# Kernel tuning notes

Hardware: AMD Instinct MI355X
Metric: run time of the kernel (lower is better)

The kernel has to match this reference:

```python
import jax, jax.numpy as jnp
import numpy as np

FP, DP, K, S, B, T, H, ZD = 96, 28, 3, 4, 64, 8, 512, 2
CP = FP - DP + 1          # 69, valid cross-correlation output size
NP = CP * CP              # 4761 = num_pixels


def setup_inputs() -> dict:
    key = jax.random.key(0)
    ks = jax.random.split(key, 12)
    def rn(k, shape, s=0.02):
        return jax.random.normal(k, shape, jnp.float32) * s
    return {
        "frames": jax.random.uniform(ks[0], (S, B, T, FP, FP), jnp.float32),
        "conv_kernel": jax.random.uniform(ks[1], (S, B, K, DP, DP), jnp.float32),
        "eps": jax.random.normal(ks[2], (S, B, K, ZD), jnp.float32),
        "W1": rn(ks[3], (NP, H)), "b1": jnp.zeros((H,), jnp.float32),
        "Wm1": rn(ks[4], (H, H // 2)), "bm1": jnp.zeros((H // 2,), jnp.float32),
        "Wm2": rn(ks[5], (H // 2, ZD)), "bm2": jnp.zeros((ZD,), jnp.float32),
        "Ws1": rn(ks[6], (H, H // 2)), "bs1": jnp.zeros((H // 2,), jnp.float32),
        "Ws2": rn(ks[7], (H // 2, ZD)), "bs2": jnp.zeros((ZD,), jnp.float32),
        "timestep": 0,
    }


def _axis_weights(p, n):
    """Bilinear 1-D gather indices/weights with zero padding outside [0, n)."""
    p0 = jnp.floor(p)
    f = p - p0
    i0 = p0.astype(jnp.int32)
    i1 = i0 + 1
    w0 = jnp.where((i0 >= 0) & (i0 < n), 1.0 - f, 0.0)
    w1 = jnp.where((i1 >= 0) & (i1 < n), f, 0.0)
    return jnp.clip(i0, 0, n - 1), jnp.clip(i1, 0, n - 1), w0, w1


def _place_digit(digit, zw):
    """AT.digit_to_frame: place DPxDP digit into FPxFP frame at z_where (torch
    affine_grid/grid_sample, align_corners=False, zero padding). theta scale =
    FP/DP, translation = -z_where*FP/DP, i.e. in_coord = (FP/DP)*(out - zw)."""
    scale = FP / DP
    out_c = (2.0 * jnp.arange(FP, dtype=jnp.float32) + 1.0) / FP - 1.0  # (FP,)
    px = ((scale * (out_c - zw[0]) + 1.0) * DP - 1.0) * 0.5  # x source pix
    py = ((scale * (out_c - zw[1]) + 1.0) * DP - 1.0) * 0.5  # y source pix
    y0, y1, wy0, wy1 = _axis_weights(py, DP)
    x0, x1, wx0, wx1 = _axis_weights(px, DP)
    # separable bilinear: interp rows then cols
    tmp = wy0[:, None] * digit[y0, :] + wy1[:, None] * digit[y1, :]  # (FP,DP)
    return wx0[None, :] * tmp[:, x0] + wx1[None, :] * tmp[:, x1]     # (FP,FP)

_place_batch = jax.vmap(_place_digit)


def reference(frames, conv_kernel, eps, W1, b1, Wm1, bm1, Wm2, bm2,
              Ws1, bs1, Ws2, bs2, timestep):
    SB = S * B
    frame_left = frames[:, :, timestep]  # (S,B,FP,FP)
    means, stds, zs = [], [], []
    for k in range(K):
        # per-sample dynamic-kernel cross-correlation via grouped conv
        lhs = frame_left.reshape(1, SB, FP, FP)
        rhs = conv_kernel[:, :, k].reshape(SB, 1, DP, DP)
        conved = jax.lax.conv_general_dilated(
            lhs, rhs, (1, 1), 'VALID', feature_group_count=SB)  # (1,SB,CP,CP)
        scores = jax.nn.softmax(conved.reshape(S, B, NP), axis=-1)
        h = jax.nn.relu(scores @ W1 + b1)                       # (S,B,H)
        mean_k = jnp.tanh(jax.nn.relu(h @ Wm1 + bm1) @ Wm2 + bm2)
        std_k = jnp.exp(jax.nn.relu(h @ Ws1 + bs1) @ Ws2 + bs2)
        z_k = mean_k + std_k * eps[:, :, k]                     # rsample
        recon = _place_batch(conv_kernel[:, :, k].reshape(SB, DP, DP),
                             z_k.reshape(SB, ZD)).reshape(S, B, FP, FP)
        frame_left = frame_left - recon
        means.append(mean_k); stds.append(std_k); zs.append(z_k)
    q_mean = jnp.stack(means, 2)    # (S,B,K,2)
    q_std = jnp.stack(stds, 2)
    z_where = jnp.stack(zs, 2)
    return jnp.stack([q_mean, q_std, z_where], 0)  # (3,S,B,K,2)
```

## Files before the change

kernel.cpp:

```cpp
#include <hip/hip_runtime.h>
#include <hip/hip_bf16.h>
#include <math.h>

#define FPD 96
#define DPD 28
#define CPD 69
#define NPD 4761
#define KKC 3
#define SBN 256
#define TT 8
#define HD 512
#define ZDD 2
#define KPAD 4768
#define SPLITK 15
#define FRSH 104
#define CVS 76

typedef __attribute__((ext_vector_type(8))) short bf16x8;
typedef __attribute__((ext_vector_type(4))) float f32x4;
typedef _Float16 half_t;
typedef __attribute__((ext_vector_type(2))) _Float16 half2_t;

__device__ __forceinline__ float bf2f_lo(unsigned int u) {
    union { unsigned int i; float f; } v; v.i = u << 16; return v.f;
}
__device__ __forceinline__ float bf2f_hi(unsigned int u) {
    union { unsigned int i; float f; } v; v.i = u & 0xffff0000u; return v.f;
}
__device__ __forceinline__ half2_t u2h(unsigned int u) {
    union { unsigned int i; half2_t h; } v; v.i = u; return v.h;
}

__global__ __launch_bounds__(256) void wprep_kernel(
    const float* __restrict__ W1, const float* __restrict__ Wm1,
    const float* __restrict__ Ws1,
    ushort* __restrict__ W1T, ushort* __restrict__ WhidT)
{
    __shared__ ushort tile[64][65];
    const int t = threadIdx.x;
    const int ln = t & 63;
    const int lr = t >> 6;
    const int b = blockIdx.x;

    if (b < 600) {
        const int k0 = (b % 75) * 64;
        const int n0 = (b / 75) * 64;
        #pragma unroll
        for (int i = 0; i < 16; ++i) {
            int kk = k0 + lr + i * 4;
            float v = (kk < NPD) ? W1[(size_t)kk * HD + n0 + ln] : 0.f;
            __hip_bfloat16 h = __float2bfloat16(v);
            tile[lr + i * 4][ln] = *reinterpret_cast<ushort*>(&h);
        }
        __syncthreads();
        #pragma unroll
        for (int i = 0; i < 16; ++i) {
            int nn = lr + i * 4;
            int kk = k0 + ln;
            if (kk < KPAD)
                W1T[(size_t)(n0 + nn) * KPAD + kk] = tile[ln][nn];
        }
    } else {
        const int bb = b - 600;
        const int i0 = (bb & 7) * 64;
        const int r0 = (bb >> 3) * 64;
        #pragma unroll
        for (int rep = 0; rep < 16; ++rep) {
            int i = i0 + lr + rep * 4;
            int r = r0 + ln;
            const float* src = (r >= 256) ? Ws1 : Wm1;
            float v = src[(size_t)i * 256 + (r & 255)];
            __hip_bfloat16 h = __float2bfloat16(v);
            tile[lr + rep * 4][ln] = *reinterpret_cast<ushort*>(&h);
        }
        __syncthreads();
        #pragma unroll
        for (int rep = 0; rep < 16; ++rep) {
            int r = r0 + lr + rep * 4;
            WhidT[(size_t)r * 512 + i0 + ln] = tile[ln][lr + rep * 4];
        }
    }
}

__global__ __launch_bounds__(1024, 4) void conv_softmax_kernel(
    const float* __restrict__ frames, const int* __restrict__ tsp,
    float* __restrict__ frameL, const float* __restrict__ ck,
    const float* __restrict__ z_cur,
    ushort* __restrict__ e_buf, float* __restrict__ inv_denom, int k)
{
    __shared__ __align__(16) half_t fr[96 * FRSH];
    __shared__ __align__(16) half_t kr[28 * 32];
    __shared__ float dg[784];
    __shared__ __align__(16) float cv[4][69 * CVS];
    __shared__ float red[32];

    const int t = threadIdx.x;
    const int ib = blockIdx.x;

    if (t < 28 * 32) {
        int dy = t >> 5, dx = t & 31;
        float v = (dx < 28) ? ck[((size_t)ib * KKC + k) * 784 + dy * 28 + dx] : 0.f;
        kr[t] = (half_t)v;
    }
    if (k > 0 && t < 784) dg[t] = ck[((size_t)ib * KKC + (k - 1)) * 784 + t];
    float zx = 0.f, zy = 0.f;
    if (k > 0) { zx = z_cur[ib * 2]; zy = z_cur[ib * 2 + 1]; }
    __syncthreads();

    const float* src = (k < 2)
        ? frames + ((size_t)ib * TT + *tsp) * 9216
        : frameL + (size_t)ib * 9216;
    const float scale = 96.f / 28.f;
    for (int p = t; p < 9216; p += 1024) {
        int r = p / 96, c = p - r * 96;
        float val = src[p];
        if (k > 0) {
            float oci = (2.f * r + 1.f) / 96.f - 1.f;
            float ocj = (2.f * c + 1.f) / 96.f - 1.f;
            float py = ((scale * (oci - zy) + 1.f) * 28.f - 1.f) * 0.5f;
            float px = ((scale * (ocj - zx) + 1.f) * 28.f - 1.f) * 0.5f;
            float py0f = floorf(py), px0f = floorf(px);
            float fy = py - py0f, fx = px - px0f;
            int y0 = (int)py0f, x0 = (int)px0f;
            int y1 = y0 + 1, x1 = x0 + 1;
            float wy0 = (y0 >= 0 && y0 < DPD) ? 1.f - fy : 0.f;
            float wy1 = (y1 >= 0 && y1 < DPD) ? fy : 0.f;
            float wx0 = (x0 >= 0 && x0 < DPD) ? 1.f - fx : 0.f;
            float wx1 = (x1 >= 0 && x1 < DPD) ? fx : 0.f;
            int y0c = min(max(y0, 0), DPD - 1), y1c = min(max(y1, 0), DPD - 1);
            int x0c = min(max(x0, 0), DPD - 1), x1c = min(max(x1, 0), DPD - 1);
            float tmp0 = wy0 * dg[y0c * DPD + x0c] + wy1 * dg[y1c * DPD + x0c];
            float tmp1 = wy0 * dg[y0c * DPD + x1c] + wy1 * dg[y1c * DPD + x1c];
            val -= wx0 * tmp0 + wx1 * tmp1;
        }
        fr[r * FRSH + c] = (half_t)val;
        if (k == 1) frameL[(size_t)ib * 9216 + p] = val;
    }
    if (t < 96 * 8) fr[(t >> 3) * FRSH + 96 + (t & 7)] = (half_t)0.f;
    __syncthreads();

    if (t < 828) {
        const int q    = t / 207;
        const int rem  = t - q * 207;
        const int tile = rem / 69;
        const int oy   = rem - tile * 69;
        const int ox0  = tile * 24;
        const int dy0  = q * 7;

        float acc[24];
        #pragma unroll
        for (int j = 0; j < 24; ++j) acc[j] = 0.f;

        #pragma unroll 1
        for (int dd = 0; dd < 7; ++dd) {
            const int dy = dy0 + dd;
            const unsigned int* frow = (const unsigned int*)&fr[(oy + dy) * FRSH + ox0];
            const unsigned int* krow = (const unsigned int*)&kr[dy * 32];
            unsigned int W[28], K[16], V[25];
            #pragma unroll
            for (int u = 0; u < 7; ++u) {
                uint4 v = *(const uint4*)(frow + 4 * u);
                W[4*u] = v.x; W[4*u+1] = v.y; W[4*u+2] = v.z; W[4*u+3] = v.w;
            }
            #pragma unroll
            for (int u = 0; u < 4; ++u) {
                uint4 v = *(const uint4*)(krow + 4 * u);
                K[4*u] = v.x; K[4*u+1] = v.y; K[4*u+2] = v.z; K[4*u+3] = v.w;
            }
            #pragma unroll
            for (int i = 0; i < 25; ++i)
                V[i] = (W[i] >> 16) | (W[i + 1] << 16);
            #pragma unroll
            for (int m = 0; m < 12; ++m) {
                float ae = acc[2*m], ao = acc[2*m+1];
                #pragma unroll
                for (int i = 0; i < 14; ++i) {
                    ae = __builtin_amdgcn_fdot2(u2h(W[m + i]), u2h(K[i]), ae, false);
                    ao = __builtin_amdgcn_fdot2(u2h(V[m + i]), u2h(K[i]), ao, false);
                }
                acc[2*m] = ae; acc[2*m+1] = ao;
            }
        }
        float* cvq = &cv[q][oy * CVS + ox0];
        #pragma unroll
        for (int u = 0; u < 6; ++u) {
            float4 v = make_float4(acc[4*u], acc[4*u+1], acc[4*u+2], acc[4*u+3]);
            *(float4*)(cvq + 4 * u) = v;
        }
    }
    __syncthreads();

    float m = -INFINITY;
    for (int p = t; p < 69 * CVS; p += 1024) {
        int ox = p - (p / CVS) * CVS;
        if (ox < CPD) {
            float v = cv[0][p] + cv[1][p] + cv[2][p] + cv[3][p];
            cv[0][p] = v;
            m = fmaxf(m, v);
        }
    }
    #pragma unroll
    for (int off = 32; off > 0; off >>= 1) m = fmaxf(m, __shfl_down(m, off, 64));
    int lane = t & 63, wid = t >> 6;
    if (lane == 0) red[wid] = m;
    __syncthreads();
    m = red[0];
    #pragma unroll
    for (int i = 1; i < 16; ++i) m = fmaxf(m, red[i]);

    float s = 0.f;
    ushort* eo = e_buf + (size_t)ib * KPAD;
    for (int p = t; p < 69 * CVS; p += 1024) {
        int oy = p / CVS;
        int ox = p - oy * CVS;
        if (ox < CPD) {
            float ev = __expf(cv[0][p] - m);
            __hip_bfloat16 h = __float2bfloat16(ev);
            eo[oy * CPD + ox] = *reinterpret_cast<ushort*>(&h);
            s += ev;
        }
    }
    #pragma unroll
    for (int off = 32; off > 0; off >>= 1) s += __shfl_down(s, off, 64);
    if (lane == 0) red[16 + wid] = s;
    __syncthreads();
    if (t == 0) {
        float tot = 0.f;
        #pragma unroll
        for (int i = 0; i < 16; ++i) tot += red[16 + i];
        inv_denom[ib] = 1.0f / tot;
    }
    if (t < KPAD - NPD) eo[NPD + t] = 0;
}

__global__ __launch_bounds__(256) void gemm1_mfma(
    const ushort* __restrict__ E, const ushort* __restrict__ W1T,
    float* __restrict__ Cpart)
{
    __shared__ __align__(16) ushort As[64][56];
    __shared__ __align__(16) ushort Bs[64][56];

    const int t  = threadIdx.x;
    const int m0 = blockIdx.x * 64;
    const int n0 = blockIdx.y * 64;
    const int z  = blockIdx.z;
    const int step0 = z * 10;
    const int nstep = min(10, 149 - step0);

    const int r = t >> 2;
    const int c = t & 3;
    const int l = t & 63;
    const int w = t >> 6;
    const int lm = l & 15;
    const int kb = l >> 4;

    f32x4 zero = {0.f, 0.f, 0.f, 0.f};
    f32x4 acc[4] = {zero, zero, zero, zero};

    const ushort* eA = E   + (size_t)(m0 + r) * KPAD + c * 8;
    const ushort* eB = W1T + (size_t)(n0 + r) * KPAD + c * 8;

    int k0 = step0 * 32;
    float4 av = *(const float4*)(eA + k0);
    float4 bv = *(const float4*)(eB + k0);

    for (int s = 0; s < nstep; ++s) {
        *(float4*)&As[r][c * 8] = av;
        *(float4*)&Bs[r][c * 8] = bv;
        __syncthreads();
        if (s + 1 < nstep) {
            int kn = (step0 + s + 1) * 32;
            av = *(const float4*)(eA + kn);
            bv = *(const float4*)(eB + kn);
        }
        bf16x8 a = *(const bf16x8*)&As[w * 16 + lm][kb * 8];
        #pragma unroll
        for (int j = 0; j < 4; ++j) {
            bf16x8 b = *(const bf16x8*)&Bs[j * 16 + lm][kb * 8];
            acc[j] = __builtin_amdgcn_mfma_f32_16x16x32_bf16(a, b, acc[j], 0, 0, 0);
        }
        __syncthreads();
    }

    const int mrow = m0 + w * 16 + kb * 4;
    #pragma unroll
    for (int j = 0; j < 4; ++j) {
        int n = n0 + j * 16 + lm;
        #pragma unroll
        for (int rg = 0; rg < 4; ++rg)
            Cpart[((size_t)z * SBN + mrow + rg) * HD + n] = acc[j][rg];
    }
}

__global__ __launch_bounds__(512) void mlp_fused(
    const float* __restrict__ Cpart, const float* __restrict__ inv_denom,
    const float* __restrict__ b1, const ushort* __restrict__ WhidT,
    const float* __restrict__ bm1, const float* __restrict__ bs1,
    const float* __restrict__ Wm2, const float* __restrict__ bm2,
    const float* __restrict__ Ws2, const float* __restrict__ bs2,
    const float* __restrict__ eps, float* __restrict__ out,
    float* __restrict__ z_cur, int k)
{
    __shared__ float hsh[HD];
    __shared__ float h2[2][256];
    __shared__ float res_sh[2][2];

    const int t = threadIdx.x;
    const int ib = blockIdx.x;

    {
        float s = 0.f;
        #pragma unroll
        for (int z = 0; z < SPLITK; ++z)
            s += Cpart[((size_t)z * SBN + ib) * HD + t];
        hsh[t] = fmaxf(fmaf(s, inv_denom[ib], b1[t]), 0.f);
    }
    __syncthreads();

    {
        int head = t >> 8, col = t & 255;
        const uint4* Wr = (const uint4*)(WhidT + (size_t)(head * 256 + col) * 512);
        float bias = head ? bs1[col] : bm1[col];
        float a = 0.f;
        #pragma unroll 8
        for (int u = 0; u < 64; ++u) {
            uint4 wv = Wr[u];
            const float* hp = &hsh[u * 8];
            a = fmaf(hp[0], bf2f_lo(wv.x), a);
            a = fmaf(hp[1], bf2f_hi(wv.x), a);
            a = fmaf(hp[2], bf2f_lo(wv.y), a);
            a = fmaf(hp[3], bf2f_hi(wv.y), a);
            a = fmaf(hp[4], bf2f_lo(wv.z), a);
            a = fmaf(hp[5], bf2f_hi(wv.z), a);
            a = fmaf(hp[6], bf2f_lo(wv.w), a);
            a = fmaf(hp[7], bf2f_hi(wv.w), a);
        }
        h2[head][col] = fmaxf(a + bias, 0.f);
    }
    __syncthreads();

    {
        int w = t >> 6, l = t & 63;
        if (w < 4) {
            int zd = (w >> 1) & 1, head = w & 1;
            const float* W2 = head ? Ws2 : Wm2;
            float a = 0.f;
            #pragma unroll
            for (int u = 0; u < 4; ++u) {
                int i = l + u * 64;
                a = fmaf(h2[head][i], W2[i * 2 + zd], a);
            }
            #pragma unroll
            for (int off = 32; off > 0; off >>= 1) a += __shfl_down(a, off, 64);
            if (l == 0) {
                float r = head ? __expf(a + bs2[zd]) : tanhf(a + bm2[zd]);
                res_sh[zd][head] = r;
            }
        }
    }
    __syncthreads();
    if (t < 2) {
        int zd = t;
        float mean = res_sh[zd][0];
        float stdv = res_sh[zd][1];
        float ev = eps[(size_t)ib * 6 + k * 2 + zd];
        float z = fmaf(stdv, ev, mean);
        int oidx = ib * 6 + k * 2 + zd;
        out[oidx]        = mean;
        out[1536 + oidx] = stdv;
        out[3072 + oidx] = z;
        z_cur[ib * 2 + zd] = z;
    }
}

extern "C" void kernel_launch(void* const* d_in, const int* in_sizes, int n_in,
                              void* d_out, int out_size, void* d_ws, size_t ws_size,
                              hipStream_t stream)
{
    const float* frames = (const float*)d_in[0];
    const float* ck     = (const float*)d_in[1];
    const float* eps    = (const float*)d_in[2];
    const float* W1     = (const float*)d_in[3];
    const float* b1     = (const float*)d_in[4];
    const float* Wm1    = (const float*)d_in[5];
    const float* bm1    = (const float*)d_in[6];
    const float* Wm2    = (const float*)d_in[7];
    const float* bm2    = (const float*)d_in[8];
    const float* Ws1    = (const float*)d_in[9];
    const float* bs1    = (const float*)d_in[10];
    const float* Ws2    = (const float*)d_in[11];
    const float* bs2    = (const float*)d_in[12];
    const int*   tsp    = (const int*)d_in[13];
    float* out = (float*)d_out;

    float* frameL  = (float*)d_ws;
    float* Cpart   = frameL + 2359296;
    float* inv_den = Cpart + 1966080;
    float* z_cur   = inv_den + 256;
    ushort* e_buf  = (ushort*)(z_cur + 512);
    ushort* W1T    = e_buf + (size_t)SBN * KPAD;
    ushort* WhidT  = W1T + (size_t)HD * KPAD;

    wprep_kernel<<<664, 256, 0, stream>>>(W1, Wm1, Ws1, W1T, WhidT);

    for (int k = 0; k < KKC; ++k) {
        conv_softmax_kernel<<<256, 1024, 0, stream>>>(
            frames, tsp, frameL, ck, z_cur, e_buf, inv_den, k);
        gemm1_mfma<<<dim3(4, 8, SPLITK), 256, 0, stream>>>(e_buf, W1T, Cpart);
        mlp_fused<<<256, 512, 0, stream>>>(Cpart, inv_den, b1, WhidT,
                                           bm1, bs1, Wm2, bm2, Ws2, bs2,
                                           eps, out, z_cur, k);
    }
}
```

Measured before the change: 301.1 us.

## Fuse weight prep into first conv and MLP into next conv stage

Folds the weight transpose/bf16 conversion into the first conv+softmax kernel as a tail phase, and merges each MLP step with the following step's conv+softmax in one 1024-thread kernel, sharing LDS through a union. This cuts the launch count from 10 to 7 and passes z through shared memory instead of a global buffer. The cost is that the MLP phase now runs in 1024-thread blocks with half the threads idle, and the bigger fused kernels may lower occupancy or lengthen their critical path.

New measurement: 297.9 us. About the same (-1.1%).

```diff
diff --git a/kernel.cpp b/kernel.cpp
--- a/kernel.cpp
+++ b/kernel.cpp
@@ -31,71 +31,31 @@
     union { unsigned int i; half2_t h; } v; v.i = u; return v.h;
 }
 
-__global__ __launch_bounds__(256) void wprep_kernel(
-    const float* __restrict__ W1, const float* __restrict__ Wm1,
-    const float* __restrict__ Ws1,
-    ushort* __restrict__ W1T, ushort* __restrict__ WhidT)
-{
-    __shared__ ushort tile[64][65];
-    const int t = threadIdx.x;
-    const int ln = t & 63;
-    const int lr = t >> 6;
-    const int b = blockIdx.x;
-
-    if (b < 600) {
-        const int k0 = (b % 75) * 64;
-        const int n0 = (b / 75) * 64;
-        #pragma unroll
-        for (int i = 0; i < 16; ++i) {
-            int kk = k0 + lr + i * 4;
-            float v = (kk < NPD) ? W1[(size_t)kk * HD + n0 + ln] : 0.f;
-            __hip_bfloat16 h = __float2bfloat16(v);
-            tile[lr + i * 4][ln] = *reinterpret_cast<ushort*>(&h);
-        }
-        __syncthreads();
-        #pragma unroll
-        for (int i = 0; i < 16; ++i) {
-            int nn = lr + i * 4;
-            int kk = k0 + ln;
-            if (kk < KPAD)
-                W1T[(size_t)(n0 + nn) * KPAD + kk] = tile[ln][nn];
-        }
-    } else {
-        const int bb = b - 600;
-        const int i0 = (bb & 7) * 64;
-        const int r0 = (bb >> 3) * 64;
-        #pragma unroll
-        for (int rep = 0; rep < 16; ++rep) {
-            int i = i0 + lr + rep * 4;
-            int r = r0 + ln;
-            const float* src = (r >= 256) ? Ws1 : Wm1;
-            float v = src[(size_t)i * 256 + (r & 255)];
-            __hip_bfloat16 h = __float2bfloat16(v);
-            tile[lr + rep * 4][ln] = *reinterpret_cast<ushort*>(&h);
-        }
-        __syncthreads();
-        #pragma unroll
-        for (int rep = 0; rep < 16; ++rep) {
-            int r = r0 + lr + rep * 4;
-            WhidT[(size_t)r * 512 + i0 + ln] = tile[ln][lr + rep * 4];
-        }
-    }
-}
-
-__global__ __launch_bounds__(1024, 4) void conv_softmax_kernel(
+struct ConvLds {
+    half_t fr[96 * FRSH];
+    half_t kr[28 * 32];
+    float  dg[784];
+    float  cv[4][69 * CVS];
+    float  red[32];
+};
+
+struct MlpLds {
+    float hsh[HD];
+    float h2[2][256];
+    float res_sh[2][2];
+};
+
+__device__ __forceinline__ void conv_phase(
+    ConvLds& L, int k, int ib, int t,
     const float* __restrict__ frames, const int* __restrict__ tsp,
     float* __restrict__ frameL, const float* __restrict__ ck,
-    const float* __restrict__ z_cur,
-    ushort* __restrict__ e_buf, float* __restrict__ inv_denom, int k)
-{
-    __shared__ __align__(16) half_t fr[96 * FRSH];
-    __shared__ __align__(16) half_t kr[28 * 32];
-    __shared__ float dg[784];
-    __shared__ __align__(16) float cv[4][69 * CVS];
-    __shared__ float red[32];
-
-    const int t = threadIdx.x;
-    const int ib = blockIdx.x;
+    float zx, float zy,
+    ushort* __restrict__ e_buf, float* __restrict__ inv_denom)
+{
+    half_t* fr  = L.fr;
+    half_t* kr  = L.kr;
+    float*  dg  = L.dg;
+    float*  red = L.red;
 
     if (t < 28 * 32) {
         int dy = t >> 5, dx = t & 31;
@@ -103,8 +63,6 @@
         kr[t] = (half_t)v;
     }
     if (k > 0 && t < 784) dg[t] = ck[((size_t)ib * KKC + (k - 1)) * 784 + t];
-    float zx = 0.f, zy = 0.f;
-    if (k > 0) { zx = z_cur[ib * 2]; zy = z_cur[ib * 2 + 1]; }
     __syncthreads();
 
     const float* src = (k < 2)
@@ -181,7 +139,7 @@
                 acc[2*m] = ae; acc[2*m+1] = ao;
             }
         }
-        float* cvq = &cv[q][oy * CVS + ox0];
+        float* cvq = &L.cv[q][oy * CVS + ox0];
         #pragma unroll
         for (int u = 0; u < 6; ++u) {
             float4 v = make_float4(acc[4*u], acc[4*u+1], acc[4*u+2], acc[4*u+3]);
@@ -194,8 +152,8 @@
     for (int p = t; p < 69 * CVS; p += 1024) {
         int ox = p - (p / CVS) * CVS;
         if (ox < CPD) {
-            float v = cv[0][p] + cv[1][p] + cv[2][p] + cv[3][p];
-            cv[0][p] = v;
+            float v = L.cv[0][p] + L.cv[1][p] + L.cv[2][p] + L.cv[3][p];
+            L.cv[0][p] = v;
             m = fmaxf(m, v);
         }
     }
@@ -214,7 +172,7 @@
         int oy = p / CVS;
         int ox = p - oy * CVS;
         if (ox < CPD) {
-            float ev = __expf(cv[0][p] - m);
+            float ev = __expf(L.cv[0][p] - m);
             __hip_bfloat16 h = __float2bfloat16(ev);
             eo[oy * CPD + ox] = *reinterpret_cast<ushort*>(&h);
             s += ev;
@@ -231,6 +189,81 @@
         inv_denom[ib] = 1.0f / tot;
     }
     if (t < KPAD - NPD) eo[NPD + t] = 0;
+}
+
+__global__ __launch_bounds__(1024, 4) void conv0_wprep_kernel(
+    const float* __restrict__ frames, const int* __restrict__ tsp,
+    float* __restrict__ frameL, const float* __restrict__ ck,
+    ushort* __restrict__ e_buf, float* __restrict__ inv_denom,
+    const float* __restrict__ W1, const float* __restrict__ Wm1,
+    const float* __restrict__ Ws1,
+    ushort* __restrict__ W1T, ushort* __restrict__ WhidT)
+{
+    __shared__ union __align__(16) {
+        ConvLds conv;
+        ushort wp[4][64][65];
+    } sh;
+    const int t  = threadIdx.x;
+    const int ib = blockIdx.x;
+
+    conv_phase(sh.conv, 0, ib, t, frames, tsp, frameL, ck, 0.f, 0.f,
+               e_buf, inv_denom);
+    __syncthreads();
+
+    {
+        const int g  = t >> 8;
+        const int tt = t & 255;
+        const int ln = tt & 63;
+        const int lr = tt >> 6;
+        const int b  = ib * 4 + g;
+        ushort (*tile)[65] = sh.wp[g];
+
+        if (b < 600) {
+            const int k0 = (b % 75) * 64;
+            const int n0 = (b / 75) * 64;
+            #pragma unroll
+            for (int i = 0; i < 16; ++i) {
+                int kk = k0 + lr + i * 4;
+                float v = (kk < NPD) ? W1[(size_t)kk * HD + n0 + ln] : 0.f;
+                __hip_bfloat16 h = __float2bfloat16(v);
+                tile[lr + i * 4][ln] = *reinterpret_cast<ushort*>(&h);
+            }
+        } else if (b < 664) {
+            const int bb = b - 600;
+            const int i0 = (bb & 7) * 64;
+            const int r0 = (bb >> 3) * 64;
+            #pragma unroll
+            for (int rep = 0; rep < 16; ++rep) {
+                int i = i0 + lr + rep * 4;
+                int r = r0 + ln;
+                const float* srcp = (r >= 256) ? Ws1 : Wm1;
+                float v = srcp[(size_t)i * 256 + (r & 255)];
+                __hip_bfloat16 h = __float2bfloat16(v);
+                tile[lr + rep * 4][ln] = *reinterpret_cast<ushort*>(&h);
+            }
+        }
+        __syncthreads();
+        if (b < 600) {
+            const int k0 = (b % 75) * 64;
+            const int n0 = (b / 75) * 64;
+            #pragma unroll
+            for (int i = 0; i < 16; ++i) {
+                int nn = lr + i * 4;
+                int kk = k0 + ln;
+                if (kk < KPAD)
+                    W1T[(size_t)(n0 + nn) * KPAD + kk] = tile[ln][nn];
+            }
+        } else if (b < 664) {
+            const int bb = b - 600;
+            const int i0 = (bb & 7) * 64;
+            const int r0 = (bb >> 3) * 64;
+            #pragma unroll
+            for (int rep = 0; rep < 16; ++rep) {
+                int r = r0 + lr + rep * 4;
+                WhidT[(size_t)r * 512 + i0 + ln] = tile[ln][lr + rep * 4];
+            }
+        }
+    }
 }
 
 __global__ __launch_bounds__(256) void gemm1_mfma(
@@ -292,32 +325,26 @@
     }
 }
 
-__global__ __launch_bounds__(512) void mlp_fused(
+__device__ __forceinline__ void mlp_phase(
+    MlpLds& L, int km, int ib, int t,
     const float* __restrict__ Cpart, const float* __restrict__ inv_denom,
     const float* __restrict__ b1, const ushort* __restrict__ WhidT,
     const float* __restrict__ bm1, const float* __restrict__ bs1,
     const float* __restrict__ Wm2, const float* __restrict__ bm2,
     const float* __restrict__ Ws2, const float* __restrict__ bs2,
     const float* __restrict__ eps, float* __restrict__ out,
-    float* __restrict__ z_cur, int k)
-{
-    __shared__ float hsh[HD];
-    __shared__ float h2[2][256];
-    __shared__ float res_sh[2][2];
-
-    const int t = threadIdx.x;
-    const int ib = blockIdx.x;
-
-    {
+    float* z_keep)
+{
+    if (t < HD) {
         float s = 0.f;
         #pragma unroll
         for (int z = 0; z < SPLITK; ++z)
             s += Cpart[((size_t)z * SBN + ib) * HD + t];
-        hsh[t] = fmaxf(fmaf(s, inv_denom[ib], b1[t]), 0.f);
-    }
-    __syncthreads();
-
-    {
+        L.hsh[t] = fmaxf(fmaf(s, inv_denom[ib], b1[t]), 0.f);
+    }
+    __syncthreads();
+
+    if (t < 512) {
         int head = t >> 8, col = t & 255;
         const uint4* Wr = (const uint4*)(WhidT + (size_t)(head * 256 + col) * 512);
         float bias = head ? bs1[col] : bm1[col];
@@ -325,7 +352,7 @@
         #pragma unroll 8
         for (int u = 0; u < 64; ++u) {
             uint4 wv = Wr[u];
-            const float* hp = &hsh[u * 8];
+            const float* hp = &L.hsh[u * 8];
             a = fmaf(hp[0], bf2f_lo(wv.x), a);
             a = fmaf(hp[1], bf2f_hi(wv.x), a);
             a = fmaf(hp[2], bf2f_lo(wv.y), a);
@@ -335,7 +362,7 @@
             a = fmaf(hp[6], bf2f_lo(wv.w), a);
             a = fmaf(hp[7], bf2f_hi(wv.w), a);
         }
-        h2[head][col] = fmaxf(a + bias, 0.f);
+        L.h2[head][col] = fmaxf(a + bias, 0.f);
     }
     __syncthreads();
 
@@ -348,29 +375,71 @@
             #pragma unroll
             for (int u = 0; u < 4; ++u) {
                 int i = l + u * 64;
-                a = fmaf(h2[head][i], W2[i * 2 + zd], a);
+                a = fmaf(L.h2[head][i], W2[i * 2 + zd], a);
             }
             #pragma unroll
             for (int off = 32; off > 0; off >>= 1) a += __shfl_down(a, off, 64);
             if (l == 0) {
                 float r = head ? __expf(a + bs2[zd]) : tanhf(a + bm2[zd]);
-                res_sh[zd][head] = r;
+                L.res_sh[zd][head] = r;
             }
         }
     }
     __syncthreads();
     if (t < 2) {
         int zd = t;
-        float mean = res_sh[zd][0];
-        float stdv = res_sh[zd][1];
-        float ev = eps[(size_t)ib * 6 + k * 2 + zd];
+        float mean = L.res_sh[zd][0];
+        float stdv = L.res_sh[zd][1];
+        float ev = eps[(size_t)ib * 6 + km * 2 + zd];
         float z = fmaf(stdv, ev, mean);
-        int oidx = ib * 6 + k * 2 + zd;
+        int oidx = ib * 6 + km * 2 + zd;
         out[oidx]        = mean;
         out[1536 + oidx] = stdv;
         out[3072 + oidx] = z;
-        z_cur[ib * 2 + zd] = z;
-    }
+        z_keep[zd] = z;
+    }
+}
+
+__global__ __launch_bounds__(1024, 4) void mlp_conv_kernel(
+    const float* __restrict__ Cpart, const float* __restrict__ inv_denom,
+    const float* __restrict__ b1, const ushort* __restrict__ WhidT,
+    const float* __restrict__ bm1, const float* __restrict__ bs1,
+    const float* __restrict__ Wm2, const float* __restrict__ bm2,
+    const float* __restrict__ Ws2, const float* __restrict__ bs2,
+    const float* __restrict__ eps, float* __restrict__ out,
+    const float* __restrict__ frames, const int* __restrict__ tsp,
+    float* __restrict__ frameL, const float* __restrict__ ck,
+    ushort* __restrict__ e_buf, int km)
+{
+    __shared__ union __align__(16) {
+        ConvLds conv;
+        MlpLds  mlp;
+    } sh;
+    __shared__ float z_keep[2];
+    const int t  = threadIdx.x;
+    const int ib = blockIdx.x;
+
+    mlp_phase(sh.mlp, km, ib, t, Cpart, inv_denom, b1, WhidT,
+              bm1, bs1, Wm2, bm2, Ws2, bs2, eps, out, z_keep);
+    __syncthreads();
+
+    float zx = z_keep[0], zy = z_keep[1];
+    conv_phase(sh.conv, km + 1, ib, t, frames, tsp, frameL, ck, zx, zy,
+               e_buf, (float*)inv_denom);
+}
+
+__global__ __launch_bounds__(512) void mlp_final_kernel(
+    const float* __restrict__ Cpart, const float* __restrict__ inv_denom,
+    const float* __restrict__ b1, const ushort* __restrict__ WhidT,
+    const float* __restrict__ bm1, const float* __restrict__ bs1,
+    const float* __restrict__ Wm2, const float* __restrict__ bm2,
+    const float* __restrict__ Ws2, const float* __restrict__ bs2,
+    const float* __restrict__ eps, float* __restrict__ out)
+{
+    __shared__ MlpLds L;
+    __shared__ float z_keep[2];
+    mlp_phase(L, 2, blockIdx.x, threadIdx.x, Cpart, inv_denom, b1, WhidT,
+              bm1, bs1, Wm2, bm2, Ws2, bs2, eps, out, z_keep);
 }
 
 extern "C" void kernel_launch(void* const* d_in, const int* in_sizes, int n_in,
@@ -396,19 +465,21 @@
     float* frameL  = (float*)d_ws;
     float* Cpart   = frameL + 2359296;
     float* inv_den = Cpart + 1966080;
-    float* z_cur   = inv_den + 256;
-    ushort* e_buf  = (ushort*)(z_cur + 512);
+    ushort* e_buf  = (ushort*)(inv_den + 256);
     ushort* W1T    = e_buf + (size_t)SBN * KPAD;
     ushort* WhidT  = W1T + (size_t)HD * KPAD;
 
-    wprep_kernel<<<664, 256, 0, stream>>>(W1, Wm1, Ws1, W1T, WhidT);
-
-    for (int k = 0; k < KKC; ++k) {
-        conv_softmax_kernel<<<256, 1024, 0, stream>>>(
-            frames, tsp, frameL, ck, z_cur, e_buf, inv_den, k);
-        gemm1_mfma<<<dim3(4, 8, SPLITK), 256, 0, stream>>>(e_buf, W1T, Cpart);
-        mlp_fused<<<256, 512, 0, stream>>>(Cpart, inv_den, b1, WhidT,
-                                           bm1, bs1, Wm2, bm2, Ws2, bs2,
-                                           eps, out, z_cur, k);
-    }
-}
+    conv0_wprep_kernel<<<256, 1024, 0, stream>>>(
+        frames, tsp, frameL, ck, e_buf, inv_den, W1, Wm1, Ws1, W1T, WhidT);
+    gemm1_mfma<<<dim3(4, 8, SPLITK), 256, 0, stream>>>(e_buf, W1T, Cpart);
+    mlp_conv_kernel<<<256, 1024, 0, stream>>>(
+        Cpart, inv_den, b1, WhidT, bm1, bs1, Wm2, bm2, Ws2, bs2,
+        eps, out, frames, tsp, frameL, ck, e_buf, 0);
+    gemm1_mfma<<<dim3(4, 8, SPLITK), 256, 0, stream>>>(e_buf, W1T, Cpart);
+    mlp_conv_kernel<<<256, 1024, 0, stream>>>(
+        Cpart, inv_den, b1, WhidT, bm1, bs1, Wm2, bm2, Ws2, bs2,
+        eps, out, frames, tsp, frameL, ck, e_buf, 1);
+    gemm1_mfma<<<dim3(4, 8, SPLITK), 256, 0, stream>>>(e_buf, W1T, Cpart);
+    mlp_final_kernel<<<256, 512, 0, stream>>>(
+        Cpart, inv_den, b1, WhidT, bm1, bs1, Wm2, bm2, Ws2, bs2, eps, out);
+}
```
